# Kernel optimization log

Measured on AMD Instinct MI355X. Metric: run time of the kernel, lower is better.

## Reference

```python
import jax, jax.numpy as jnp
import numpy as np

E = 128
H = 4
D = E // H  # head dim = 32
NEG = -1e9


def setup_inputs() -> dict:
    key = jax.random.key(0)
    ks = jax.random.split(key, 4)
    B, N = 8, 2048
    x = jax.random.normal(ks[0], (B, N, E), dtype=jnp.float32)
    adj = jax.random.randint(ks[1], (B, N, N), 0, 2, dtype=jnp.int32)
    # nn.MultiheadAttention params: packed in_proj (3E,E) + out_proj (E,E)
    in_proj_w = jax.random.normal(ks[2], (3 * E, E), dtype=jnp.float32) * (1.0 / np.sqrt(E))
    in_proj_b = jnp.zeros((3 * E,), dtype=jnp.float32)
    out_w = jax.random.normal(ks[3], (E, E), dtype=jnp.float32) * (1.0 / np.sqrt(E))
    out_b = jnp.zeros((E,), dtype=jnp.float32)
    return {"x": x, "adj": adj, "in_proj_w": in_proj_w, "in_proj_b": in_proj_b,
            "out_w": out_w, "out_b": out_b}


def reference(x, adj, in_proj_w, in_proj_b, out_w, out_b):
    B, N, _ = x.shape
    # additive mask from FIRST batch element only (as in the torch module)
    mask = jnp.where(adj[0] == 0, jnp.float32(NEG), jnp.float32(0.0))  # (N,N)
    # packed QKV projection: x @ W^T + b
    qkv = x @ in_proj_w.T + in_proj_b  # (B,N,3E)
    q, k, v = jnp.split(qkv, 3, axis=-1)
    # (B,N,E) -> (B,H,N,D)
    def heads(t):
        return t.reshape(B, N, H, D).transpose(0, 2, 1, 3)
    q, k, v = heads(q), heads(k), heads(v)
    scores = jnp.einsum('bhnd,bhmd->bhnm', q, k) / jnp.sqrt(jnp.float32(D))
    scores = scores + mask[None, None]  # broadcast shared mask
    attn = jax.nn.softmax(scores, axis=-1)
    out = jnp.einsum('bhnm,bhmd->bhnd', attn, v)  # (B,H,N,D)
    out = out.transpose(0, 2, 1, 3).reshape(B, N, E)
    return out @ out_w.T + out_b
```

## Files before the change

kernel.cpp:

```cpp
#include <hip/hip_runtime.h>


#define EDIM 128
#define SCALE2 0.25503483f
#define COFF  -5.7707801f

typedef unsigned int uint32;
typedef float f32x4 __attribute__((ext_vector_type(4)));
typedef short s16x8 __attribute__((ext_vector_type(8)));
typedef _Float16 f16x2 __attribute__((ext_vector_type(2)));
typedef _Float16 f16x4 __attribute__((ext_vector_type(4)));
typedef _Float16 f16x8 __attribute__((ext_vector_type(8)));
typedef __fp16 g16x2 __attribute__((ext_vector_type(2)));

__device__ inline float bf2f(ushort u) { return __uint_as_float(((uint32)u) << 16); }
__device__ inline ushort f2bf(float f) {
  uint32 u = __float_as_uint(f);
  u += 0x7fffu + ((u >> 16) & 1u);
  return (ushort)(u >> 16);
}
__device__ inline uint32 packbf(float a, float b) {
  uint32 ua = __float_as_uint(a) + 0x8000u;
  uint32 ub = __float_as_uint(b) + 0x8000u;
  return __builtin_amdgcn_perm(ub, ua, 0x07060302u);
}
__device__ inline f16x2 pkrtz(float a, float b) {
  g16x2 t = __builtin_amdgcn_cvt_pkrtz(a, b);
  return __builtin_bit_cast(f16x2, t);
}
__device__ inline float fexp2(float x) {
#if __has_builtin(__builtin_amdgcn_exp2f)
  return __builtin_amdgcn_exp2f(x);
#else
  return __exp2f(x);
#endif
}

__device__ inline f32x4 mfma32(s16x8 a, s16x8 b, f32x4 c) {
  return __builtin_amdgcn_mfma_f32_16x16x32_bf16(a, b, c, 0, 0, 0);
}
__device__ inline f32x4 mfma32h(f16x8 a, f16x8 b, f32x4 c) {
  return __builtin_amdgcn_mfma_f32_16x16x32_f16(a, b, c, 0, 0, 0);
}

__device__ inline int sniff_fp32(const ushort* __restrict__ xus) {
  int lane = threadIdx.x & 63, cnt = 0;
#pragma unroll
  for (int i = 0; i < 4; i++) {
    ushort v = xus[2 * (lane * 4 + i)];
    int ex = (v >> 7) & 0xFF;
    cnt += (ex >= 100 && ex <= 140) ? 1 : 0;
  }
#pragma unroll
  for (int s = 1; s < 64; s <<= 1) cnt += __shfl_xor(cnt, s);
  return cnt < 128;
}

__device__ inline s16x8 load8(const void* p, size_t e, int fp32) {
  if (fp32) {
    const float* f = (const float*)p + e;
    float4 lo = *(const float4*)f;
    float4 hi = *(const float4*)(f + 4);
    union { s16x8 s; uint32 u[4]; } r;
    r.u[0] = packbf(lo.x, lo.y);
    r.u[1] = packbf(lo.z, lo.w);
    r.u[2] = packbf(hi.x, hi.y);
    r.u[3] = packbf(hi.z, hi.w);
    return r.s;
  }
  return *(const s16x8*)((const ushort*)p + e);
}
__device__ inline float loads(const void* p, size_t e, int fp32) {
  return fp32 ? ((const float*)p)[e] : bf2f(((const ushort*)p)[e]);
}

__global__ __launch_bounds__(256) void k_pre(const void* __restrict__ x,
                                             const void* __restrict__ w,
                                             const void* __restrict__ bias,
                                             ushort* __restrict__ Qg,
                                             ushort* __restrict__ Kg,
                                             _Float16* __restrict__ Vth,
                                             const int4* __restrict__ adj4,
                                             uint32* __restrict__ mb) {
  if (blockIdx.y >= 6) {
    int g = ((blockIdx.y - 6) * 256 + blockIdx.x) * 256 + threadIdx.x;
    int4 v = adj4[g];
    int lane = threadIdx.x & 63;
    uint32 nib = (v.x != 0 ? 1u : 0u) | (v.y != 0 ? 2u : 0u) |
                 (v.z != 0 ? 4u : 0u) | (v.w != 0 ? 8u : 0u);
    uint32 wbit = nib << (4 * (lane & 7));
    wbit |= __shfl_xor(wbit, 1);
    wbit |= __shfl_xor(wbit, 2);
    wbit |= __shfl_xor(wbit, 4);
    if ((lane & 7) == 0) mb[g >> 3] = wbit;
    return;
  }

  const int fp32 = sniff_fp32((const ushort*)x);
  const int tid = threadIdx.x;
  const int wave = tid >> 6, lane = tid & 63, L = lane & 15, quad = lane >> 4;
  const int mt = blockIdx.x * 64 + wave * 16;
  const int jt0 = blockIdx.y * 4;

  s16x8 a[4];
#pragma unroll
  for (int ks = 0; ks < 4; ks++)
    a[ks] = load8(x, (size_t)(mt + L) * EDIM + ks * 32 + quad * 8, fp32);

  const int bidx = mt >> 11;
  const int npos0 = (mt & 2047) + quad * 4;

  for (int jj = 0; jj < 4; jj++) {
    int jt = jt0 + jj;
    f32x4 acc = {0.f, 0.f, 0.f, 0.f};
#pragma unroll
    for (int ks = 0; ks < 4; ks++) {
      s16x8 bf = load8(w, (size_t)(jt * 16 + L) * EDIM + ks * 32 + quad * 8, fp32);
      acc = mfma32(a[ks], bf, acc);
    }
    int j = jt * 16 + L;
    float badd = loads(bias, j, fp32);
    int jm = j & 127;
    int h = jm >> 5, d = jm & 31;
    int bh = bidx * 4 + h;
    int ch = npos0 >> 7, kk = npos0 & 127;
    if (jt < 8) {
#pragma unroll
      for (int r = 0; r < 4; r++)
        Qg[(size_t)bh * 65536 + (size_t)(npos0 + r) * 32 + d] = f2bf((acc[r] + badd) * SCALE2);
    } else if (jt < 16) {
      int sub = kk >> 5, k32 = kk & 31, t = k32 >> 3, r8 = k32 & 7;
      int slot0 = sub * 32 + ((r8 >> 2) << 4) + t * 4;
      size_t kb = (size_t)bh * 65536 + (size_t)ch * 4096;
#pragma unroll
      for (int r = 0; r < 4; r++)
        Kg[kb + (size_t)(slot0 + r) * 32 + (((d >> 3) ^ r) << 3) + (d & 7)] =
            f2bf(acc[r] + badd);
    } else {
      int g = kk >> 3, e0 = kk & 7;
      f16x2 h0 = pkrtz(acc[0] + badd, acc[1] + badd);
      f16x2 h1 = pkrtz(acc[2] + badd, acc[3] + badd);
      f16x4 pk; pk[0] = h0[0]; pk[1] = h0[1]; pk[2] = h1[0]; pk[3] = h1[1];
      *(f16x4*)(Vth + (size_t)bh * 65536 + (size_t)ch * 4096 + d * 128 +
                (g ^ (d & 7)) * 8 + e0) = pk;
    }
  }
}

__global__ __launch_bounds__(512, 4) void k_attn(const ushort* __restrict__ Qg,
                                                 const ushort* __restrict__ Kg,
                                                 const _Float16* __restrict__ Vth,
                                                 const uint32* __restrict__ mb,
                                                 ushort* __restrict__ Oa) {
  __shared__ float cb[4352];

  const int tid = threadIdx.x;
  const int wv = tid >> 6, lane = tid & 63, L = lane & 15, quad = lane >> 4;
  const int half = wv >> 2, wl = wv & 3;
  const int bid = blockIdx.x;
  const int bh = ((bid >> 3) & 3) * 8 + (bid & 7);
  const int qc = bid >> 5;
  const int q0 = qc * 128 + wl * 32;
  const int qgA = q0 + L, qgB = q0 + 16 + L;

  const ushort* Qb = Qg + (size_t)bh * 65536;
  s16x8 qfA = *(const s16x8*)(Qb + (size_t)qgA * 32 + quad * 8);
  s16x8 qfB = *(const s16x8*)(Qb + (size_t)qgB * 32 + quad * 8);

  f32x4 OA0 = {0,0,0,0}, OA1 = {0,0,0,0}, OB0 = {0,0,0,0}, OB1 = {0,0,0,0};
  f32x4 LA = {0,0,0,0}, LB = {0,0,0,0};
  f16x8 ones;
#pragma unroll
  for (int i = 0; i < 8; i++) ones[i] = (_Float16)1.0f;

  const char* Kg8 = (const char*)(Kg + (size_t)bh * 65536) + (size_t)half * 65536;
  const char* Vg8 = (const char*)(Vth + (size_t)bh * 65536) + (size_t)half * 65536;
  const int g0 = quad ^ (L & 3);

  const char* kA = Kg8 + L * 64 + g0 * 16;
  const char* vA = Vg8 + L * 256;
  const uint32* mbA = mb + (size_t)qgA * 64 + half * 32;
  const uint32* mbB = mb + (size_t)qgB * 64 + half * 32;

#define LOADT(T, K0, K1, V0, V1)                                             \
  do {                                                                       \
    const int cc_ = (T) >> 2, sub_ = (T) & 3;                                \
    K0 = *(const s16x8*)(kA + cc_ * 8192 + sub_ * 2048);                     \
    K1 = *(const s16x8*)(kA + cc_ * 8192 + sub_ * 2048 + 1024);              \
    const int vg_ = (sub_ * 4 + quad) ^ (L & 7);                             \
    V0 = *(const f16x8*)(vA + cc_ * 8192 + vg_ * 16);                        \
    V1 = *(const f16x8*)(vA + cc_ * 8192 + 4096 + vg_ * 16);                 \
  } while (0)

#define MW4(M, S) ((S) == 0 ? (M).x : (S) == 1 ? (M).y : (S) == 2 ? (M).z : (M).w)

  s16x8 ck0, ck1, nk0, nk1, tk0, tk1;
  f16x8 cv0, cv1, nv0, nv1, tv0, tv1;
  uint4 mcA, mcB, mnA, mnB;

  LOADT(0, ck0, ck1, cv0, cv1);
  LOADT(1, nk0, nk1, nv0, nv1);
  mcA = *(const uint4*)mbA;
  mcB = *(const uint4*)mbB;
  tk0 = nk0; tk1 = nk1; tv0 = nv0; tv1 = nv1;
  mnA = mcA; mnB = mcB;

#pragma unroll
  for (int t = 0; t < 32; ++t) {
    const int cc = t >> 2, sub = t & 3;
    if (sub == 0 && cc + 1 < 8) {
      mnA = *(const uint4*)(mbA + (cc + 1) * 4);
      mnB = *(const uint4*)(mbB + (cc + 1) * 4);
    }
    if (t + 2 < 32) LOADT(t + 2, tk0, tk1, tv0, tv1);

    {
      const f32x4 Zc = {COFF, COFF, COFF, COFF};
      f32x4 sA0 = mfma32(ck0, qfA, Zc), sA1 = mfma32(ck1, qfA, Zc);
      f32x4 sB0 = mfma32(ck0, qfB, Zc), sB1 = mfma32(ck1, qfB, Zc);

      uint32 mwqA = MW4(mcA, sub) >> (quad * 8);
      uint32 mwqB = MW4(mcB, sub) >> (quad * 8);
      union { f16x8 v; f16x2 h[4]; } pA, pB;
      float a0 = ((mwqA >> 0) & 1u) ? fexp2(sA0[0]) : 0.f;
      float a1 = ((mwqA >> 1) & 1u) ? fexp2(sA0[1]) : 0.f;
      float a2 = ((mwqA >> 2) & 1u) ? fexp2(sA0[2]) : 0.f;
      float a3 = ((mwqA >> 3) & 1u) ? fexp2(sA0[3]) : 0.f;
      float a4 = ((mwqA >> 4) & 1u) ? fexp2(sA1[0]) : 0.f;
      float a5 = ((mwqA >> 5) & 1u) ? fexp2(sA1[1]) : 0.f;
      float a6 = ((mwqA >> 6) & 1u) ? fexp2(sA1[2]) : 0.f;
      float a7 = ((mwqA >> 7) & 1u) ? fexp2(sA1[3]) : 0.f;
      pA.h[0] = pkrtz(a0, a1); pA.h[1] = pkrtz(a2, a3);
      pA.h[2] = pkrtz(a4, a5); pA.h[3] = pkrtz(a6, a7);
      float b0 = ((mwqB >> 0) & 1u) ? fexp2(sB0[0]) : 0.f;
      float b1 = ((mwqB >> 1) & 1u) ? fexp2(sB0[1]) : 0.f;
      float b2 = ((mwqB >> 2) & 1u) ? fexp2(sB0[2]) : 0.f;
      float b3 = ((mwqB >> 3) & 1u) ? fexp2(sB0[3]) : 0.f;
      float b4 = ((mwqB >> 4) & 1u) ? fexp2(sB1[0]) : 0.f;
      float b5 = ((mwqB >> 5) & 1u) ? fexp2(sB1[1]) : 0.f;
      float b6 = ((mwqB >> 6) & 1u) ? fexp2(sB1[2]) : 0.f;
      float b7 = ((mwqB >> 7) & 1u) ? fexp2(sB1[3]) : 0.f;
      pB.h[0] = pkrtz(b0, b1); pB.h[1] = pkrtz(b2, b3);
      pB.h[2] = pkrtz(b4, b5); pB.h[3] = pkrtz(b6, b7);

      OA0 = mfma32h(cv0, pA.v, OA0);  OA1 = mfma32h(cv1, pA.v, OA1);
      OB0 = mfma32h(cv0, pB.v, OB0);  OB1 = mfma32h(cv1, pB.v, OB1);
      LA  = mfma32h(ones, pA.v, LA);  LB  = mfma32h(ones, pB.v, LB);
    }

    ck0 = nk0; ck1 = nk1; cv0 = nv0; cv1 = nv1;
    nk0 = tk0; nk1 = tk1; nv0 = tv0; nv1 = tv1;
    if (sub == 3) { mcA = mnA; mcB = mnB; }
  }

  __syncthreads();
  const int cbase = wl * 1088;
  if (half) {
#pragma unroll
    for (int r = 0; r < 4; r++) {
      cb[cbase + L * 33 + quad * 4 + r]             = OA0[r];
      cb[cbase + L * 33 + 16 + quad * 4 + r]        = OA1[r];
      cb[cbase + (16 + L) * 33 + quad * 4 + r]      = OB0[r];
      cb[cbase + (16 + L) * 33 + 16 + quad * 4 + r] = OB1[r];
    }
    if (quad == 0) {
      cb[cbase + 1056 + L]      = LA[0];
      cb[cbase + 1056 + 16 + L] = LB[0];
    }
  }
  __syncthreads();
  if (!half) {
#pragma unroll
    for (int r = 0; r < 4; r++) {
      OA0[r] += cb[cbase + L * 33 + quad * 4 + r];
      OA1[r] += cb[cbase + L * 33 + 16 + quad * 4 + r];
      OB0[r] += cb[cbase + (16 + L) * 33 + quad * 4 + r];
      OB1[r] += cb[cbase + (16 + L) * 33 + 16 + quad * 4 + r];
    }
    float rnA = 1.0f / (LA[0] + cb[cbase + 1056 + L]);
    float rnB = 1.0f / (LB[0] + cb[cbase + 1056 + 16 + L]);
    int b = bh >> 2, h = bh & 3;
    {
      size_t ob = ((size_t)(b * 2048 + qgA)) * 128 + h * 32 + quad * 4;
      ushort4 p0, p1;
      p0.x = f2bf(OA0[0] * rnA); p0.y = f2bf(OA0[1] * rnA);
      p0.z = f2bf(OA0[2] * rnA); p0.w = f2bf(OA0[3] * rnA);
      p1.x = f2bf(OA1[0] * rnA); p1.y = f2bf(OA1[1] * rnA);
      p1.z = f2bf(OA1[2] * rnA); p1.w = f2bf(OA1[3] * rnA);
      *(ushort4*)(Oa + ob) = p0; *(ushort4*)(Oa + ob + 16) = p1;
    }
    {
      size_t ob = ((size_t)(b * 2048 + qgB)) * 128 + h * 32 + quad * 4;
      ushort4 p0, p1;
      p0.x = f2bf(OB0[0] * rnB); p0.y = f2bf(OB0[1] * rnB);
      p0.z = f2bf(OB0[2] * rnB); p0.w = f2bf(OB0[3] * rnB);
      p1.x = f2bf(OB1[0] * rnB); p1.y = f2bf(OB1[1] * rnB);
      p1.z = f2bf(OB1[2] * rnB); p1.w = f2bf(OB1[3] * rnB);
      *(ushort4*)(Oa + ob) = p0; *(ushort4*)(Oa + ob + 16) = p1;
    }
  }
}

__global__ __launch_bounds__(256) void k_proj(void* outp, const ushort* Oa,
                                              const void* w, const void* bias,
                                              const ushort* __restrict__ xus) {
  const int fp32 = sniff_fp32(xus);
  const ushort* src = Oa;
  const int tid = threadIdx.x;
  const int wave = tid >> 6, lane = tid & 63, L = lane & 15, quad = lane >> 4;
  const int mt = blockIdx.x * 64 + wave * 16;
  const int jt0 = blockIdx.y * 2;

  s16x8 a[4];
#pragma unroll
  for (int ks = 0; ks < 4; ks++)
    a[ks] = *(const s16x8*)(src + (size_t)(mt + L) * EDIM + ks * 32 + quad * 8);

  for (int jt = jt0; jt < jt0 + 2; jt++) {
    f32x4 acc = {0.f, 0.f, 0.f, 0.f};
#pragma unroll
    for (int ks = 0; ks < 4; ks++) {
      s16x8 bf = load8(w, (size_t)(jt * 16 + L) * EDIM + ks * 32 + quad * 8, fp32);
      acc = mfma32(a[ks], bf, acc);
    }
    float badd = loads(bias, jt * 16 + L, fp32);
#pragma unroll
    for (int r = 0; r < 4; r++) {
      size_t idx = (size_t)(mt + quad * 4 + r) * EDIM + jt * 16 + L;
      if (fp32) ((float*)outp)[idx] = acc[r] + badd;
      else      ((ushort*)outp)[idx] = f2bf(acc[r] + badd);
    }
  }
}

extern "C" void kernel_launch(void* const* d_in, const int* in_sizes, int n_in,
                              void* d_out, int out_size, void* d_ws, size_t ws_size,
                              hipStream_t stream) {
  const void* x   = d_in[0];
  const int*  adj = (const int*)d_in[1];
  const void* ipw = d_in[2];
  const void* ipb = d_in[3];
  const void* ow  = d_in[4];
  const void* ob  = d_in[5];

  char* ws = (char*)d_ws;
  ushort*   Qg  = (ushort*)(ws);
  ushort*   Kg  = (ushort*)(ws + ((size_t)4 << 20));
  _Float16* Vth = (_Float16*)(ws + ((size_t)8 << 20));
  uint32*   mb  = (uint32*)(ws + ((size_t)12 << 20));
  ushort*   Oa  = (ushort*)(ws + ((size_t)13 << 20));

  hipLaunchKernelGGL(k_pre, dim3(256, 22), dim3(256), 0, stream, x, ipw, ipb,
                     Qg, Kg, Vth, (const int4*)adj, mb);
  hipLaunchKernelGGL(k_attn, dim3(512), dim3(512), 0, stream, Qg, Kg, Vth, mb,
                     Oa);
  hipLaunchKernelGGL(k_proj, dim3(256, 4), dim3(256), 0, stream, d_out, Oa, ow, ob,
                     (const ushort*)x);
}
```

Baseline: 245.2 us.

## Fuse pre, attention and projection into one cooperative kernel with grid syncs

Merges the three launches (mask packing plus QKV projection, attention, output projection) into one cooperative kernel of 512 blocks, separated by grid-wide barriers. The work of each phase is remapped onto the 512 blocks of 512 threads. This is meant to remove the launch overhead and tail gaps between kernels. In exchange it adds two grid.sync barriers, changes the per-block work split in the projection phases, and keeps the old three-kernel path as a fallback if the cooperative launch fails.

```diff
diff --git a/kernel.cpp b/kernel.cpp
--- a/kernel.cpp
+++ b/kernel.cpp
@@ -1,4 +1,7 @@
 #include <hip/hip_runtime.h>
+#include <hip/hip_cooperative_groups.h>
+
+namespace cg = cooperative_groups;
 
 
 #define EDIM 128
@@ -72,6 +75,271 @@
 }
 __device__ inline float loads(const void* p, size_t e, int fp32) {
   return fp32 ? ((const float*)p)[e] : bf2f(((const ushort*)p)[e]);
+}
+
+__device__ inline void qkv_store(int jt, int L, int quad, int mt, f32x4 acc,
+                                 float badd, ushort* __restrict__ Qg,
+                                 ushort* __restrict__ Kg,
+                                 _Float16* __restrict__ Vth) {
+  int j = jt * 16 + L;
+  int jm = j & 127;
+  int h = jm >> 5, d = jm & 31;
+  int bidx = mt >> 11;
+  int npos0 = (mt & 2047) + quad * 4;
+  int bh = bidx * 4 + h;
+  int ch = npos0 >> 7, kk = npos0 & 127;
+  if (jt < 8) {
+#pragma unroll
+    for (int r = 0; r < 4; r++)
+      Qg[(size_t)bh * 65536 + (size_t)(npos0 + r) * 32 + d] = f2bf((acc[r] + badd) * SCALE2);
+  } else if (jt < 16) {
+    int sub = kk >> 5, k32 = kk & 31, t = k32 >> 3, r8 = k32 & 7;
+    int slot0 = sub * 32 + ((r8 >> 2) << 4) + t * 4;
+    size_t kb = (size_t)bh * 65536 + (size_t)ch * 4096;
+#pragma unroll
+    for (int r = 0; r < 4; r++)
+      Kg[kb + (size_t)(slot0 + r) * 32 + (((d >> 3) ^ r) << 3) + (d & 7)] =
+          f2bf(acc[r] + badd);
+  } else {
+    int g = kk >> 3, e0 = kk & 7;
+    f16x2 h0 = pkrtz(acc[0] + badd, acc[1] + badd);
+    f16x2 h1 = pkrtz(acc[2] + badd, acc[3] + badd);
+    f16x4 pk; pk[0] = h0[0]; pk[1] = h0[1]; pk[2] = h1[0]; pk[3] = h1[1];
+    *(f16x4*)(Vth + (size_t)bh * 65536 + (size_t)ch * 4096 + d * 128 +
+              (g ^ (d & 7)) * 8 + e0) = pk;
+  }
+}
+
+__global__ __launch_bounds__(512, 4) void k_all(const void* __restrict__ x,
+                                                const void* __restrict__ w,
+                                                const void* __restrict__ bias,
+                                                ushort* __restrict__ Qg,
+                                                ushort* __restrict__ Kg,
+                                                _Float16* __restrict__ Vth,
+                                                const int4* __restrict__ adj4,
+                                                uint32* __restrict__ mb,
+                                                const void* __restrict__ ow,
+                                                const void* __restrict__ obias,
+                                                void* __restrict__ outp,
+                                                ushort* __restrict__ Oa) {
+  __shared__ float cb[4352];
+  cg::grid_group grid = cg::this_grid();
+
+  const int tid = threadIdx.x;
+  const int bid = blockIdx.x;
+  const int wv = tid >> 6, lane = tid & 63, L = lane & 15, quad = lane >> 4;
+  const int fp32 = sniff_fp32((const ushort*)x);
+
+  {
+    int gbase = bid * 2048 + tid;
+#pragma unroll
+    for (int r = 0; r < 4; r++) {
+      int g = gbase + r * 512;
+      int4 v = adj4[g];
+      uint32 nib = (v.x != 0 ? 1u : 0u) | (v.y != 0 ? 2u : 0u) |
+                   (v.z != 0 ? 4u : 0u) | (v.w != 0 ? 8u : 0u);
+      uint32 wbit = nib << (4 * (lane & 7));
+      wbit |= __shfl_xor(wbit, 1);
+      wbit |= __shfl_xor(wbit, 2);
+      wbit |= __shfl_xor(wbit, 4);
+      if ((lane & 7) == 0) mb[g >> 3] = wbit;
+    }
+  }
+
+  {
+    const int mt = bid * 32 + (wv & 1) * 16;
+    const int jt0 = (wv >> 1) * 6;
+    s16x8 a[4];
+#pragma unroll
+    for (int ks = 0; ks < 4; ks++)
+      a[ks] = load8(x, (size_t)(mt + L) * EDIM + ks * 32 + quad * 8, fp32);
+    for (int jj = 0; jj < 6; jj++) {
+      int jt = jt0 + jj;
+      f32x4 acc = {0.f, 0.f, 0.f, 0.f};
+#pragma unroll
+      for (int ks = 0; ks < 4; ks++) {
+        s16x8 bf = load8(w, (size_t)(jt * 16 + L) * EDIM + ks * 32 + quad * 8, fp32);
+        acc = mfma32(a[ks], bf, acc);
+      }
+      float badd = loads(bias, jt * 16 + L, fp32);
+      qkv_store(jt, L, quad, mt, acc, badd, Qg, Kg, Vth);
+    }
+  }
+
+  grid.sync();
+
+  {
+    const int half = wv >> 2, wl = wv & 3;
+    const int bh = ((bid >> 3) & 3) * 8 + (bid & 7);
+    const int qc = bid >> 5;
+    const int q0 = qc * 128 + wl * 32;
+    const int qgA = q0 + L, qgB = q0 + 16 + L;
+
+    const ushort* Qb = Qg + (size_t)bh * 65536;
+    s16x8 qfA = *(const s16x8*)(Qb + (size_t)qgA * 32 + quad * 8);
+    s16x8 qfB = *(const s16x8*)(Qb + (size_t)qgB * 32 + quad * 8);
+
+    f32x4 OA0 = {0,0,0,0}, OA1 = {0,0,0,0}, OB0 = {0,0,0,0}, OB1 = {0,0,0,0};
+    f32x4 LA = {0,0,0,0}, LB = {0,0,0,0};
+    f16x8 ones;
+#pragma unroll
+    for (int i = 0; i < 8; i++) ones[i] = (_Float16)1.0f;
+
+    const char* Kg8 = (const char*)(Kg + (size_t)bh * 65536) + (size_t)half * 65536;
+    const char* Vg8 = (const char*)(Vth + (size_t)bh * 65536) + (size_t)half * 65536;
+    const int g0 = quad ^ (L & 3);
+
+    const char* kA = Kg8 + L * 64 + g0 * 16;
+    const char* vA = Vg8 + L * 256;
+    const uint32* mbA = mb + (size_t)qgA * 64 + half * 32;
+    const uint32* mbB = mb + (size_t)qgB * 64 + half * 32;
+
+#define LOADT(T, K0, K1, V0, V1)                                             \
+  do {                                                                       \
+    const int cc_ = (T) >> 2, sub_ = (T) & 3;                                \
+    K0 = *(const s16x8*)(kA + cc_ * 8192 + sub_ * 2048);                     \
+    K1 = *(const s16x8*)(kA + cc_ * 8192 + sub_ * 2048 + 1024);              \
+    const int vg_ = (sub_ * 4 + quad) ^ (L & 7);                             \
+    V0 = *(const f16x8*)(vA + cc_ * 8192 + vg_ * 16);                        \
+    V1 = *(const f16x8*)(vA + cc_ * 8192 + 4096 + vg_ * 16);                 \
+  } while (0)
+
+#define MW4(M, S) ((S) == 0 ? (M).x : (S) == 1 ? (M).y : (S) == 2 ? (M).z : (M).w)
+
+    s16x8 ck0, ck1, nk0, nk1, tk0, tk1;
+    f16x8 cv0, cv1, nv0, nv1, tv0, tv1;
+    uint4 mcA, mcB, mnA, mnB;
+
+    LOADT(0, ck0, ck1, cv0, cv1);
+    LOADT(1, nk0, nk1, nv0, nv1);
+    mcA = *(const uint4*)mbA;
+    mcB = *(const uint4*)mbB;
+    tk0 = nk0; tk1 = nk1; tv0 = nv0; tv1 = nv1;
+    mnA = mcA; mnB = mcB;
+
+#pragma unroll
+    for (int t = 0; t < 32; ++t) {
+      const int cc = t >> 2, sub = t & 3;
+      if (sub == 0 && cc + 1 < 8) {
+        mnA = *(const uint4*)(mbA + (cc + 1) * 4);
+        mnB = *(const uint4*)(mbB + (cc + 1) * 4);
+      }
+      if (t + 2 < 32) LOADT(t + 2, tk0, tk1, tv0, tv1);
+
+      {
+        const f32x4 Zc = {COFF, COFF, COFF, COFF};
+        f32x4 sA0 = mfma32(ck0, qfA, Zc), sA1 = mfma32(ck1, qfA, Zc);
+        f32x4 sB0 = mfma32(ck0, qfB, Zc), sB1 = mfma32(ck1, qfB, Zc);
+
+        uint32 mwqA = MW4(mcA, sub) >> (quad * 8);
+        uint32 mwqB = MW4(mcB, sub) >> (quad * 8);
+        union { f16x8 v; f16x2 h[4]; } pA, pB;
+        float a0 = ((mwqA >> 0) & 1u) ? fexp2(sA0[0]) : 0.f;
+        float a1 = ((mwqA >> 1) & 1u) ? fexp2(sA0[1]) : 0.f;
+        float a2 = ((mwqA >> 2) & 1u) ? fexp2(sA0[2]) : 0.f;
+        float a3 = ((mwqA >> 3) & 1u) ? fexp2(sA0[3]) : 0.f;
+        float a4 = ((mwqA >> 4) & 1u) ? fexp2(sA1[0]) : 0.f;
+        float a5 = ((mwqA >> 5) & 1u) ? fexp2(sA1[1]) : 0.f;
+        float a6 = ((mwqA >> 6) & 1u) ? fexp2(sA1[2]) : 0.f;
+        float a7 = ((mwqA >> 7) & 1u) ? fexp2(sA1[3]) : 0.f;
+        pA.h[0] = pkrtz(a0, a1); pA.h[1] = pkrtz(a2, a3);
+        pA.h[2] = pkrtz(a4, a5); pA.h[3] = pkrtz(a6, a7);
+        float b0 = ((mwqB >> 0) & 1u) ? fexp2(sB0[0]) : 0.f;
+        float b1 = ((mwqB >> 1) & 1u) ? fexp2(sB0[1]) : 0.f;
+        float b2 = ((mwqB >> 2) & 1u) ? fexp2(sB0[2]) : 0.f;
+        float b3 = ((mwqB >> 3) & 1u) ? fexp2(sB0[3]) : 0.f;
+        float b4 = ((mwqB >> 4) & 1u) ? fexp2(sB1[0]) : 0.f;
+        float b5 = ((mwqB >> 5) & 1u) ? fexp2(sB1[1]) : 0.f;
+        float b6 = ((mwqB >> 6) & 1u) ? fexp2(sB1[2]) : 0.f;
+        float b7 = ((mwqB >> 7) & 1u) ? fexp2(sB1[3]) : 0.f;
+        pB.h[0] = pkrtz(b0, b1); pB.h[1] = pkrtz(b2, b3);
+        pB.h[2] = pkrtz(b4, b5); pB.h[3] = pkrtz(b6, b7);
+
+        OA0 = mfma32h(cv0, pA.v, OA0);  OA1 = mfma32h(cv1, pA.v, OA1);
+        OB0 = mfma32h(cv0, pB.v, OB0);  OB1 = mfma32h(cv1, pB.v, OB1);
+        LA  = mfma32h(ones, pA.v, LA);  LB  = mfma32h(ones, pB.v, LB);
+      }
+
+      ck0 = nk0; ck1 = nk1; cv0 = nv0; cv1 = nv1;
+      nk0 = tk0; nk1 = tk1; nv0 = tv0; nv1 = tv1;
+      if (sub == 3) { mcA = mnA; mcB = mnB; }
+    }
+#undef LOADT
+#undef MW4
+
+    __syncthreads();
+    const int cbase = wl * 1088;
+    if (half) {
+#pragma unroll
+      for (int r = 0; r < 4; r++) {
+        cb[cbase + L * 33 + quad * 4 + r]             = OA0[r];
+        cb[cbase + L * 33 + 16 + quad * 4 + r]        = OA1[r];
+        cb[cbase + (16 + L) * 33 + quad * 4 + r]      = OB0[r];
+        cb[cbase + (16 + L) * 33 + 16 + quad * 4 + r] = OB1[r];
+      }
+      if (quad == 0) {
+        cb[cbase + 1056 + L]      = LA[0];
+        cb[cbase + 1056 + 16 + L] = LB[0];
+      }
+    }
+    __syncthreads();
+    if (!half) {
+#pragma unroll
+      for (int r = 0; r < 4; r++) {
+        OA0[r] += cb[cbase + L * 33 + quad * 4 + r];
+        OA1[r] += cb[cbase + L * 33 + 16 + quad * 4 + r];
+        OB0[r] += cb[cbase + (16 + L) * 33 + quad * 4 + r];
+        OB1[r] += cb[cbase + (16 + L) * 33 + 16 + quad * 4 + r];
+      }
+      float rnA = 1.0f / (LA[0] + cb[cbase + 1056 + L]);
+      float rnB = 1.0f / (LB[0] + cb[cbase + 1056 + 16 + L]);
+      int b = bh >> 2, h = bh & 3;
+      {
+        size_t ob = ((size_t)(b * 2048 + qgA)) * 128 + h * 32 + quad * 4;
+        ushort4 p0, p1;
+        p0.x = f2bf(OA0[0] * rnA); p0.y = f2bf(OA0[1] * rnA);
+        p0.z = f2bf(OA0[2] * rnA); p0.w = f2bf(OA0[3] * rnA);
+        p1.x = f2bf(OA1[0] * rnA); p1.y = f2bf(OA1[1] * rnA);
+        p1.z = f2bf(OA1[2] * rnA); p1.w = f2bf(OA1[3] * rnA);
+        *(ushort4*)(Oa + ob) = p0; *(ushort4*)(Oa + ob + 16) = p1;
+      }
+      {
+        size_t ob = ((size_t)(b * 2048 + qgB)) * 128 + h * 32 + quad * 4;
+        ushort4 p0, p1;
+        p0.x = f2bf(OB0[0] * rnB); p0.y = f2bf(OB0[1] * rnB);
+        p0.z = f2bf(OB0[2] * rnB); p0.w = f2bf(OB0[3] * rnB);
+        p1.x = f2bf(OB1[0] * rnB); p1.y = f2bf(OB1[1] * rnB);
+        p1.z = f2bf(OB1[2] * rnB); p1.w = f2bf(OB1[3] * rnB);
+        *(ushort4*)(Oa + ob) = p0; *(ushort4*)(Oa + ob + 16) = p1;
+      }
+    }
+  }
+
+  grid.sync();
+
+  {
+    const int mt = bid * 32 + (wv & 1) * 16;
+    const int jt0 = (wv >> 1) * 2;
+    s16x8 a[4];
+#pragma unroll
+    for (int ks = 0; ks < 4; ks++)
+      a[ks] = *(const s16x8*)(Oa + (size_t)(mt + L) * EDIM + ks * 32 + quad * 8);
+    for (int jt = jt0; jt < jt0 + 2; jt++) {
+      f32x4 acc = {0.f, 0.f, 0.f, 0.f};
+#pragma unroll
+      for (int ks = 0; ks < 4; ks++) {
+        s16x8 bf = load8(ow, (size_t)(jt * 16 + L) * EDIM + ks * 32 + quad * 8, fp32);
+        acc = mfma32(a[ks], bf, acc);
+      }
+      float badd = loads(obias, jt * 16 + L, fp32);
+#pragma unroll
+      for (int r = 0; r < 4; r++) {
+        size_t idx = (size_t)(mt + quad * 4 + r) * EDIM + jt * 16 + L;
+        if (fp32) ((float*)outp)[idx] = acc[r] + badd;
+        else      ((ushort*)outp)[idx] = f2bf(acc[r] + badd);
+      }
+    }
+  }
 }
 
 __global__ __launch_bounds__(256) void k_pre(const void* __restrict__ x,
@@ -95,21 +363,15 @@
     if ((lane & 7) == 0) mb[g >> 3] = wbit;
     return;
   }
-
   const int fp32 = sniff_fp32((const ushort*)x);
   const int tid = threadIdx.x;
   const int wave = tid >> 6, lane = tid & 63, L = lane & 15, quad = lane >> 4;
   const int mt = blockIdx.x * 64 + wave * 16;
   const int jt0 = blockIdx.y * 4;
-
   s16x8 a[4];
 #pragma unroll
   for (int ks = 0; ks < 4; ks++)
     a[ks] = load8(x, (size_t)(mt + L) * EDIM + ks * 32 + quad * 8, fp32);
-
-  const int bidx = mt >> 11;
-  const int npos0 = (mt & 2047) + quad * 4;
-
   for (int jj = 0; jj < 4; jj++) {
     int jt = jt0 + jj;
     f32x4 acc = {0.f, 0.f, 0.f, 0.f};
@@ -118,32 +380,8 @@
       s16x8 bf = load8(w, (size_t)(jt * 16 + L) * EDIM + ks * 32 + quad * 8, fp32);
       acc = mfma32(a[ks], bf, acc);
     }
-    int j = jt * 16 + L;
-    float badd = loads(bias, j, fp32);
-    int jm = j & 127;
-    int h = jm >> 5, d = jm & 31;
-    int bh = bidx * 4 + h;
-    int ch = npos0 >> 7, kk = npos0 & 127;
-    if (jt < 8) {
-#pragma unroll
-      for (int r = 0; r < 4; r++)
-        Qg[(size_t)bh * 65536 + (size_t)(npos0 + r) * 32 + d] = f2bf((acc[r] + badd) * SCALE2);
-    } else if (jt < 16) {
-      int sub = kk >> 5, k32 = kk & 31, t = k32 >> 3, r8 = k32 & 7;
-      int slot0 = sub * 32 + ((r8 >> 2) << 4) + t * 4;
-      size_t kb = (size_t)bh * 65536 + (size_t)ch * 4096;
-#pragma unroll
-      for (int r = 0; r < 4; r++)
-        Kg[kb + (size_t)(slot0 + r) * 32 + (((d >> 3) ^ r) << 3) + (d & 7)] =
-            f2bf(acc[r] + badd);
-    } else {
-      int g = kk >> 3, e0 = kk & 7;
-      f16x2 h0 = pkrtz(acc[0] + badd, acc[1] + badd);
-      f16x2 h1 = pkrtz(acc[2] + badd, acc[3] + badd);
-      f16x4 pk; pk[0] = h0[0]; pk[1] = h0[1]; pk[2] = h1[0]; pk[3] = h1[1];
-      *(f16x4*)(Vth + (size_t)bh * 65536 + (size_t)ch * 4096 + d * 128 +
-                (g ^ (d & 7)) * 8 + e0) = pk;
-    }
+    float badd = loads(bias, jt * 16 + L, fp32);
+    qkv_store(jt, L, quad, mt, acc, badd, Qg, Kg, Vth);
   }
 }
 
@@ -153,7 +391,6 @@
                                                  const uint32* __restrict__ mb,
                                                  ushort* __restrict__ Oa) {
   __shared__ float cb[4352];
-
   const int tid = threadIdx.x;
   const int wv = tid >> 6, lane = tid & 63, L = lane & 15, quad = lane >> 4;
   const int half = wv >> 2, wl = wv & 3;
@@ -162,26 +399,21 @@
   const int qc = bid >> 5;
   const int q0 = qc * 128 + wl * 32;
   const int qgA = q0 + L, qgB = q0 + 16 + L;
-
   const ushort* Qb = Qg + (size_t)bh * 65536;
   s16x8 qfA = *(const s16x8*)(Qb + (size_t)qgA * 32 + quad * 8);
   s16x8 qfB = *(const s16x8*)(Qb + (size_t)qgB * 32 + quad * 8);
-
   f32x4 OA0 = {0,0,0,0}, OA1 = {0,0,0,0}, OB0 = {0,0,0,0}, OB1 = {0,0,0,0};
   f32x4 LA = {0,0,0,0}, LB = {0,0,0,0};
   f16x8 ones;
 #pragma unroll
   for (int i = 0; i < 8; i++) ones[i] = (_Float16)1.0f;
-
   const char* Kg8 = (const char*)(Kg + (size_t)bh * 65536) + (size_t)half * 65536;
   const char* Vg8 = (const char*)(Vth + (size_t)bh * 65536) + (size_t)half * 65536;
   const int g0 = quad ^ (L & 3);
-
   const char* kA = Kg8 + L * 64 + g0 * 16;
   const char* vA = Vg8 + L * 256;
   const uint32* mbA = mb + (size_t)qgA * 64 + half * 32;
   const uint32* mbB = mb + (size_t)qgB * 64 + half * 32;
-
 #define LOADT(T, K0, K1, V0, V1)                                             \
   do {                                                                       \
     const int cc_ = (T) >> 2, sub_ = (T) & 3;                                \
@@ -191,20 +423,16 @@
     V0 = *(const f16x8*)(vA + cc_ * 8192 + vg_ * 16);                        \
     V1 = *(const f16x8*)(vA + cc_ * 8192 + 4096 + vg_ * 16);                 \
   } while (0)
-
 #define MW4(M, S) ((S) == 0 ? (M).x : (S) == 1 ? (M).y : (S) == 2 ? (M).z : (M).w)
-
   s16x8 ck0, ck1, nk0, nk1, tk0, tk1;
   f16x8 cv0, cv1, nv0, nv1, tv0, tv1;
   uint4 mcA, mcB, mnA, mnB;
-
   LOADT(0, ck0, ck1, cv0, cv1);
   LOADT(1, nk0, nk1, nv0, nv1);
   mcA = *(const uint4*)mbA;
   mcB = *(const uint4*)mbB;
   tk0 = nk0; tk1 = nk1; tv0 = nv0; tv1 = nv1;
   mnA = mcA; mnB = mcB;
-
 #pragma unroll
   for (int t = 0; t < 32; ++t) {
     const int cc = t >> 2, sub = t & 3;
@@ -213,12 +441,10 @@
       mnB = *(const uint4*)(mbB + (cc + 1) * 4);
     }
     if (t + 2 < 32) LOADT(t + 2, tk0, tk1, tv0, tv1);
-
     {
       const f32x4 Zc = {COFF, COFF, COFF, COFF};
       f32x4 sA0 = mfma32(ck0, qfA, Zc), sA1 = mfma32(ck1, qfA, Zc);
       f32x4 sB0 = mfma32(ck0, qfB, Zc), sB1 = mfma32(ck1, qfB, Zc);
-
       uint32 mwqA = MW4(mcA, sub) >> (quad * 8);
       uint32 mwqB = MW4(mcB, sub) >> (quad * 8);
       union { f16x8 v; f16x2 h[4]; } pA, pB;
@@ -242,17 +468,16 @@
       float b7 = ((mwqB >> 7) & 1u) ? fexp2(sB1[3]) : 0.f;
       pB.h[0] = pkrtz(b0, b1); pB.h[1] = pkrtz(b2, b3);
       pB.h[2] = pkrtz(b4, b5); pB.h[3] = pkrtz(b6, b7);
-
       OA0 = mfma32h(cv0, pA.v, OA0);  OA1 = mfma32h(cv1, pA.v, OA1);
       OB0 = mfma32h(cv0, pB.v, OB0);  OB1 = mfma32h(cv1, pB.v, OB1);
       LA  = mfma32h(ones, pA.v, LA);  LB  = mfma32h(ones, pB.v, LB);
     }
-
     ck0 = nk0; ck1 = nk1; cv0 = nv0; cv1 = nv1;
     nk0 = tk0; nk1 = tk1; nv0 = tv0; nv1 = tv1;
     if (sub == 3) { mcA = mnA; mcB = mnB; }
   }
-
+#undef LOADT
+#undef MW4
   __syncthreads();
   const int cbase = wl * 1088;
   if (half) {
@@ -310,12 +535,10 @@
   const int wave = tid >> 6, lane = tid & 63, L = lane & 15, quad = lane >> 4;
   const int mt = blockIdx.x * 64 + wave * 16;
   const int jt0 = blockIdx.y * 2;
-
   s16x8 a[4];
 #pragma unroll
   for (int ks = 0; ks < 4; ks++)
     a[ks] = *(const s16x8*)(src + (size_t)(mt + L) * EDIM + ks * 32 + quad * 8);
-
   for (int jt = jt0; jt < jt0 + 2; jt++) {
     f32x4 acc = {0.f, 0.f, 0.f, 0.f};
 #pragma unroll
@@ -350,10 +573,18 @@
   uint32*   mb  = (uint32*)(ws + ((size_t)12 << 20));
   ushort*   Oa  = (ushort*)(ws + ((size_t)13 << 20));
 
-  hipLaunchKernelGGL(k_pre, dim3(256, 22), dim3(256), 0, stream, x, ipw, ipb,
-                     Qg, Kg, Vth, (const int4*)adj, mb);
-  hipLaunchKernelGGL(k_attn, dim3(512), dim3(512), 0, stream, Qg, Kg, Vth, mb,
-                     Oa);
-  hipLaunchKernelGGL(k_proj, dim3(256, 4), dim3(256), 0, stream, d_out, Oa, ow, ob,
-                     (const ushort*)x);
-}
+  const int4* adj4 = (const int4*)adj;
+  void* args[] = {(void*)&x, (void*)&ipw, (void*)&ipb, (void*)&Qg, (void*)&Kg,
+                  (void*)&Vth, (void*)&adj4, (void*)&mb, (void*)&ow, (void*)&ob,
+                  (void*)&d_out, (void*)&Oa};
+  hipError_t err = hipLaunchCooperativeKernel((const void*)k_all, dim3(512),
+                                              dim3(512), args, 0, stream);
+  if (err != hipSuccess) {
+    hipLaunchKernelGGL(k_pre, dim3(256, 22), dim3(256), 0, stream, x, ipw, ipb,
+                       Qg, Kg, Vth, adj4, mb);
+    hipLaunchKernelGGL(k_attn, dim3(512), dim3(512), 0, stream, Qg, Kg, Vth, mb,
+                       Oa);
+    hipLaunchKernelGGL(k_proj, dim3(256, 4), dim3(256), 0, stream, d_out, Oa,
+                       ow, ob, (const ushort*)x);
+  }
+}
```

Result: slower. 395.3 us (+61.2%).
